# Performance work log

Measured on AMD Instinct MI355X. Metric: run time of the kernel, lower is better.

The kernel has to match this reference:

```python
import jax, jax.numpy as jnp
import numpy as np

N_S = 50000   # support points
N_Q = 50000   # query points
H = 32        # neighbors per query
K = 15        # kernel points
C_IN = 64
C_OUT = 64
G = 8         # group norm groups
RADIUS = 1.0
SIGMA = 0.6
EPS = 1e-5
NEG_SLOPE = 0.1


def setup_inputs() -> dict:
    key = jax.random.key(0)
    ks = jax.random.split(key, 8)
    s_feats = jax.random.normal(ks[0], (N_S, C_IN), jnp.float32)
    q_points = jax.random.uniform(ks[1], (N_Q, 3), jnp.float32)
    s_points = jax.random.uniform(ks[2], (N_S, 3), jnp.float32)
    # index N_S is the shadow (padding) neighbor
    neighbor_indices = jax.random.randint(ks[3], (N_Q, H), 0, N_S + 1)
    # kernel point dispositions: fixed points inside a ball of RADIUS
    d = jax.random.normal(ks[4], (K, 3), jnp.float32)
    d = d / jnp.linalg.norm(d, axis=1, keepdims=True)
    r = jax.random.uniform(ks[5], (K, 1), jnp.float32) ** (1.0 / 3.0)
    kernel_points = d * r * RADIUS                      # (K,3)
    weights = jax.random.normal(ks[6], (K, C_IN, C_OUT), jnp.float32) * (1.0 / np.sqrt(K * C_IN))
    bias = jax.random.normal(ks[7], (C_OUT,), jnp.float32) * 0.01
    gamma = jnp.ones((C_OUT,), jnp.float32)
    beta = jnp.zeros((C_OUT,), jnp.float32)
    return dict(s_feats=s_feats, q_points=q_points, s_points=s_points,
                neighbor_indices=neighbor_indices, kernel_points=kernel_points,
                weights=weights, bias=bias, gamma=gamma, beta=beta)


def kpconv(s_feats, q_points, s_points, neighbor_indices, kernel_points, weights, bias):
    # pad support set with shadow point (1e10) and zero features
    pad_pts = jnp.concatenate([s_points, jnp.full((1, 3), 1e10, s_points.dtype)], axis=0)
    pad_feats = jnp.concatenate([s_feats, jnp.zeros((1, s_feats.shape[1]), s_feats.dtype)], axis=0)
    nbr_pts = pad_pts[neighbor_indices] - q_points[:, None, :]              # (M,H,3)
    diff = nbr_pts[:, :, None, :] - kernel_points[None, None, :, :]         # (M,H,K,3)
    sq_d = jnp.sum(diff * diff, axis=-1)                                    # (M,H,K)
    # linear correlation influence, clamped at 0
    w = jnp.maximum(1.0 - jnp.sqrt(sq_d) / SIGMA, 0.0)                      # (M,H,K)
    nbr_feats = pad_feats[neighbor_indices]                                 # (M,H,Cin)
    weighted = jnp.einsum('mhk,mhc->mkc', w, nbr_feats)                     # (M,K,Cin)
    out = jnp.einsum('mkc,kcd->md', weighted, weights)                      # (M,Cout)
    # normalize by number of valid neighbors (feature-sum > 0 test, as in KPConv)
    nbr_num = jnp.sum(jnp.sum(nbr_feats, axis=-1) > 0, axis=-1)             # (M,)
    nbr_num = jnp.maximum(nbr_num, 1).astype(out.dtype)
    return out / nbr_num[:, None] + bias


def group_norm(x, gamma, beta):
    # matches GroupNorm wrapper: (M,C) -> (1,C,M) -> nn.GroupNorm -> (M,C)
    M, C = x.shape
    xg = x.T.reshape(G, C // G, M)                                          # (G,Cg,M)
    mean = xg.mean(axis=(1, 2), keepdims=True)
    var = xg.var(axis=(1, 2), keepdims=True)
    xn = ((xg - mean) / jnp.sqrt(var + EPS)).reshape(C, M).T                # (M,C)
    return xn * gamma + beta


def reference(s_feats, q_points, s_points, neighbor_indices, kernel_points, weights, bias, gamma, beta):
    x = kpconv(s_feats, q_points, s_points, neighbor_indices, kernel_points, weights, bias)
    x = group_norm(x, gamma, beta)
    x = jnp.where(x >= 0, x, NEG_SLOPE * x)                                 # LeakyReLU(0.1)
    return x[:, None, :]                                                    # unsqueeze(1): (M,1,Cout)
```

## Files before the change

kernel.cpp:

```cpp
#include <hip/hip_runtime.h>
#include <hip/hip_bf16.h>
#include <math.h>

#define NSUP 50000
#define NQ   50000
#define NH   32
#define NK   15
#define NG   8
#define INV_SIGMA (1.0f/0.6f)
#define GN_EPS 1e-5f
#define NEG  0.1f

#define QB   16
#define NBLK (NQ/QB)

#define OFF_ROWSUM 0
#define OFF_FB     50048
#define OFF_WB     (OFF_FB + 1600000)
#define OFF_PS     (OFF_WB + 30720)
#define OFF_PQ     (OFF_PS + NBLK*8)

typedef __attribute__((ext_vector_type(8))) short bf16x8;
typedef __attribute__((ext_vector_type(4))) float f32x4;
typedef __attribute__((ext_vector_type(4))) unsigned int u32x4;

__device__ __forceinline__ short f2bf(float x) {
    __hip_bfloat16 h = __float2bfloat16(x);
    return *reinterpret_cast<short*>(&h);
}

__global__ __launch_bounds__(256) void k_prep(const float* __restrict__ sf,
                                              float* __restrict__ rowsum,
                                              unsigned short* __restrict__ fb,
                                              const float* __restrict__ wts,
                                              unsigned short* __restrict__ wb) {
    if (blockIdx.x < 3125) {
        const int lane = threadIdx.x & 63;
        const int row  = blockIdx.x * 16 + (threadIdx.x >> 6) * 4 + (lane >> 4);
        const int c4   = lane & 15;
        const float4 v = ((const float4*)sf)[(size_t)row * 16 + c4];
        ushort4 b;
        b.x = (unsigned short)f2bf(v.x); b.y = (unsigned short)f2bf(v.y);
        b.z = (unsigned short)f2bf(v.z); b.w = (unsigned short)f2bf(v.w);
        *(ushort4*)&fb[(size_t)row * 64 + c4 * 4] = b;
        float s = v.x + v.y + v.z + v.w;
        #pragma unroll
        for (int o = 1; o <= 8; o <<= 1) s += __shfl_xor(s, o);
        if (c4 == 0) rowsum[row] = s;
    } else {
        int idx = (blockIdx.x - 3125) * 256 + threadIdx.x;
        if (idx >= 30 * 4 * 64 * 8) return;
        int j  = idx & 7;
        int l  = (idx >> 3) & 63;
        int n  = (idx >> 9) & 3;
        int ks = idx >> 11;
        int r  = ks * 32 + ((l >> 4) << 3) + j;
        int d  = n * 16 + (l & 15);
        wb[idx] = (unsigned short)f2bf(wts[(size_t)r * 64 + d]);
    }
}

__global__ __launch_bounds__(256, 5) void k_conv(
    const unsigned short* __restrict__ fb, const float* __restrict__ qpts,
    const float* __restrict__ spts,  const int*   __restrict__ nidx,
    const float* __restrict__ kpts,  const unsigned short* __restrict__ wb,
    const float* __restrict__ bias,  const float* __restrict__ rowsum,
    float* __restrict__ conv_out, float* __restrict__ part_s, float* __restrict__ part_q)
{
    __shared__ __align__(16) short wl16[16 * 968];
    __shared__ __align__(16) float kp4[16][4];
    __shared__ float rcl[16];

    const int tid  = threadIdx.x;
    const int wv   = tid >> 6;
    const int lane = tid & 63;
    const int g    = lane >> 4;
    const int c16  = lane & 15;

    if (tid < 16) {
        if (tid < NK) {
            kp4[tid][0] = kpts[tid*3+0];
            kp4[tid][1] = kpts[tid*3+1];
            kp4[tid][2] = kpts[tid*3+2];
        } else {
            kp4[tid][0] = 1e8f; kp4[tid][1] = 1e8f; kp4[tid][2] = 1e8f;
        }
        kp4[tid][3] = 0.f;
    }
    __syncthreads();

    const float kx = kp4[c16][0], ky = kp4[c16][1], kz = kp4[c16][2];

    const int qbase = blockIdx.x * QB;
    char*  WV  = (char*)wl16 + wv * 7424;
    float* XYP = (float*)WV;
    char*  FP  = WV + 2560;

    f32x4 pacc[4][4];
    #pragma unroll
    for (int a = 0; a < 4; a++)
        #pragma unroll
        for (int b = 0; b < 4; b++) pacc[a][b] = (f32x4){0.f,0.f,0.f,0.f};

    const int h    = lane & 31;
    const int half = lane >> 5;

    #pragma unroll
    for (int pp = 0; pp < 2; pp++) {
        const int qq = pp*2 + half;
        const int m  = qbase + wv*4 + qq;
        const float qx = qpts[m*3+0], qy = qpts[m*3+1], qz = qpts[m*3+2];
        const int  id  = nidx[(size_t)m * NH + h];
        const bool val = (id < NSUP);
        const int  ii  = val ? id : 0;
        const float dx = spts[ii*3+0]-qx, dy = spts[ii*3+1]-qy, dz = spts[ii*3+2]-qz;
        const float rs = rowsum[ii];
        unsigned long long bal = __ballot(val && rs > 0.f);
        int cA = __popcll(bal & 0xffffffffull); if (cA < 1) cA = 1;
        int cB = __popcll(bal >> 32);           if (cB < 1) cB = 1;
        if (lane == 0)  rcl[wv*4 + pp*2]     = 1.0f / (float)cA;
        if (lane == 32) rcl[wv*4 + pp*2 + 1] = 1.0f / (float)cB;
        const int si = (pp*64 + half*32 + h) * 5;
        XYP[si]     = val ? dx : 1e10f;
        XYP[si + 1] = dy;
        XYP[si + 2] = dz;
    }

    const int gr = lane >> 3;
    const int gs = lane & 7;
    int   idA[4], idB[4];
    u32x4 vA[4], vB[4];
    {
        const int m0 = qbase + wv*4;
        #pragma unroll
        for (int i = 0; i < 4; i++) idA[i] = nidx[(size_t)m0*NH + i*8 + gr];
        #pragma unroll
        for (int i = 0; i < 4; i++) {
            const int id2 = (idA[i] < NSUP) ? idA[i] : 0;
            vA[i] = *(const u32x4*)((const char*)fb + (size_t)id2*128 + gs*16);
        }
        const int m1 = qbase + wv*4 + 1;
        #pragma unroll
        for (int i = 0; i < 4; i++) idB[i] = nidx[(size_t)m1*NH + i*8 + gr];
    }

    #pragma unroll
    for (int q = 0; q < 4; q++) {
        const int pp = q >> 1, e = q & 1;
        u32x4* vc  = (q & 1) ? vB  : vA;
        u32x4* vn  = (q & 1) ? vA  : vB;
        int*   idn = (q & 1) ? idA : idB;
        int*   idt = (q & 1) ? idB : idA;

        #pragma unroll
        for (int i = 0; i < 4; i++)
            *(u32x4*)(FP + (i*8 + gr)*144 + ((gs ^ i) << 4)) = vc[i];

        if (q < 3) {
            #pragma unroll
            for (int i = 0; i < 4; i++) {
                const int id2 = (idn[i] < NSUP) ? idn[i] : 0;
                vn[i] = *(const u32x4*)((const char*)fb + (size_t)id2*128 + gs*16);
            }
        }
        if (q < 2) {
            const int mn = qbase + wv*4 + q + 2;
            #pragma unroll
            for (int i = 0; i < 4; i++) idt[i] = nidx[(size_t)mn*NH + i*8 + gr];
        }

        union { unsigned short u[8]; bf16x8 v; } ua;
        #pragma unroll
        for (int j = 0; j < 8; j++) {
            const int xi = (pp*64 + e*32 + g*8 + j) * 5;
            const float px = XYP[xi], py = XYP[xi+1], pz = XYP[xi+2];
            const float ex = px - kx, ey = py - ky, ez = pz - kz;
            const float sq = fmaf(ex, ex, fmaf(ey, ey, ez * ez));
            const float w  = fmaxf(1.0f - sqrtf(sq) * INV_SIGMA, 0.f);
            ua.u[j] = (unsigned short)f2bf(w);
        }

        #pragma unroll
        for (int ct = 0; ct < 4; ct++) {
            const char* vb = FP + (g*8)*144
                           + (((((ct << 1) | (c16 >> 3)) ^ g) & 7) << 4)
                           + ((c16 & 7) << 1);
            union { unsigned short u[8]; bf16x8 v; } ub;
            #pragma unroll
            for (int j = 0; j < 8; j++)
                ub.u[j] = *(const unsigned short*)(vb + j*144);
            pacc[q][ct] = __builtin_amdgcn_mfma_f32_16x16x32_bf16(ua.v, ub.v, pacc[q][ct], 0, 0, 0);
        }
    }

    __syncthreads();

    #pragma unroll
    for (int qq = 0; qq < 4; qq++) {
        #pragma unroll
        for (int ct = 0; ct < 4; ct++) {
            #pragma unroll
            for (int i = 0; i < 4; i++) {
                const int kk = g*4 + i;
                if (kk < NK)
                    wl16[(wv*4 + qq)*968 + kk*64 + ct*16 + c16] = f2bf(pacc[qq][ct][i]);
            }
        }
    }
    __syncthreads();

    f32x4 facc = (f32x4){0.f,0.f,0.f,0.f};
    const int z = lane >> 4;
    const short* ap = wl16 + c16*968 + z*8;
    const unsigned short* bp = wb + ((size_t)(wv * 64 + lane)) * 8;
    #pragma unroll 6
    for (int ks = 0; ks < 30; ks++) {
        bf16x8 a = *(const bf16x8*)(ap + ks*32);
        bf16x8 b = *(const bf16x8*)(bp + (size_t)ks*2048);
        facc = __builtin_amdgcn_mfma_f32_16x16x32_bf16(a, b, facc, 0, 0, 0);
    }

    const int   d  = wv*16 + c16;
    const float bs = bias[d];
    float gl = 0.f, gq = 0.f;
    #pragma unroll
    for (int i = 0; i < 4; i++) {
        const int row = z*4 + i;
        const float y = facc[i] * rcl[row] + bs;
        conv_out[(size_t)(qbase + row)*64 + d] = y;
        gl += y;
        gq = fmaf(y, y, gq);
    }
    #pragma unroll
    for (int msk = 1; msk <= 4; msk <<= 1) { gl += __shfl_xor(gl, msk); gq += __shfl_xor(gq, msk); }
    gl += __shfl_xor(gl, 16); gq += __shfl_xor(gq, 16);
    gl += __shfl_xor(gl, 32); gq += __shfl_xor(gq, 32);
    if ((lane & 55) == 0) {
        const int grp = wv*2 + (lane >> 3);
        part_s[(size_t)blockIdx.x * 8 + grp] = gl;
        part_q[(size_t)blockIdx.x * 8 + grp] = gq;
    }
}

__global__ __launch_bounds__(256) void k_apply(float* __restrict__ out,
                                               const float* __restrict__ part_s,
                                               const float* __restrict__ part_q,
                                               const float* __restrict__ gamma,
                                               const float* __restrict__ beta) {
    __shared__ double ds[32][8], dq[32][8];
    __shared__ float st[16];
    const int t = threadIdx.x;

    {
        const int gg = t & 7, chunk = t >> 3;
        const int per = (NBLK + 31) / 32;
        int lo = chunk * per, hi = lo + per; if (hi > NBLK) hi = NBLK;
        double s0 = 0.0, s1 = 0.0, s2 = 0.0, s3 = 0.0;
        double q0 = 0.0, q1 = 0.0, q2 = 0.0, q3 = 0.0;
        int i = lo;
        for (; i + 3 < hi; i += 4) {
            s0 += (double)part_s[(size_t)(i+0) * 8 + gg];
            s1 += (double)part_s[(size_t)(i+1) * 8 + gg];
            s2 += (double)part_s[(size_t)(i+2) * 8 + gg];
            s3 += (double)part_s[(size_t)(i+3) * 8 + gg];
            q0 += (double)part_q[(size_t)(i+0) * 8 + gg];
            q1 += (double)part_q[(size_t)(i+1) * 8 + gg];
            q2 += (double)part_q[(size_t)(i+2) * 8 + gg];
            q3 += (double)part_q[(size_t)(i+3) * 8 + gg];
        }
        for (; i < hi; i++) {
            s0 += (double)part_s[(size_t)i * 8 + gg];
            q0 += (double)part_q[(size_t)i * 8 + gg];
        }
        ds[chunk][gg] = (s0 + s1) + (s2 + s3);
        dq[chunk][gg] = (q0 + q1) + (q2 + q3);
        __syncthreads();
        if (t < 8) {
            double S = 0.0, Q = 0.0;
            for (int cix = 0; cix < 32; cix++) { S += ds[cix][t]; Q += dq[cix][t]; }
            const double cnt = (double)(64 / NG) * (double)NQ;
            double mean = S / cnt;
            double var  = Q / cnt - mean * mean;
            st[t]     = (float)mean;
            st[8 + t] = (float)(1.0 / sqrt(var + (double)GN_EPS));
        }
        __syncthreads();
    }

    const int n4 = NQ * 64 / 4;
    for (int idx = blockIdx.x * 256 + t; idx < n4; idx += gridDim.x * 256) {
        float4 v = ((const float4*)out)[idx];
        const int c4 = idx & 15;
        const int g  = c4 >> 1;
        const float mean = st[g], istd = st[8 + g];
        const float4 ga = ((const float4*)gamma)[c4];
        const float4 be = ((const float4*)beta)[c4];
        float4 r;
        r.x = (v.x - mean) * istd * ga.x + be.x; r.x = r.x >= 0.f ? r.x : NEG * r.x;
        r.y = (v.y - mean) * istd * ga.y + be.y; r.y = r.y >= 0.f ? r.y : NEG * r.y;
        r.z = (v.z - mean) * istd * ga.z + be.z; r.z = r.z >= 0.f ? r.z : NEG * r.z;
        r.w = (v.w - mean) * istd * ga.w + be.w; r.w = r.w >= 0.f ? r.w : NEG * r.w;
        ((float4*)out)[idx] = r;
    }
}

extern "C" void kernel_launch(void* const* d_in, const int* in_sizes, int n_in,
                              void* d_out, int out_size, void* d_ws, size_t ws_size,
                              hipStream_t stream) {
    const float* sfeats = (const float*)d_in[0];
    const float* qpts   = (const float*)d_in[1];
    const float* spts   = (const float*)d_in[2];
    const int*   nidx   = (const int*)  d_in[3];
    const float* kpts   = (const float*)d_in[4];
    const float* wts    = (const float*)d_in[5];
    const float* bias   = (const float*)d_in[6];
    const float* gamma  = (const float*)d_in[7];
    const float* beta   = (const float*)d_in[8];

    float* ws = (float*)d_ws;
    float*          rowsum = ws + OFF_ROWSUM;
    unsigned short* fb     = (unsigned short*)(ws + OFF_FB);
    unsigned short* wb     = (unsigned short*)(ws + OFF_WB);
    float*          ps     = ws + OFF_PS;
    float*          pq     = ws + OFF_PQ;
    float*          out    = (float*)d_out;

    k_prep <<<dim3(3365), dim3(256), 0, stream>>>(sfeats, rowsum, fb, wts, wb);
    k_conv <<<dim3(NBLK), dim3(256), 0, stream>>>(fb, qpts, spts, nidx, kpts,
                                                  wb, bias, rowsum, out, ps, pq);
    k_apply<<<dim3(512),  dim3(256), 0, stream>>>(out, ps, pq, gamma, beta);
}
```

Baseline: 76.78 us.

## Deepen neighbor feature gather prefetch to triple buffering and widen apply grid

The neighbor-feature gather pipeline in the conv kernel moves from double to triple buffering. Feature loads for the first two queries are now issued before the point-geometry setup, so their latency overlaps with that work, and later gathers are issued two stages ahead. This raises register pressure through the extra vC and idC buffers, which could lower occupancy. The group-norm apply kernel launch also grows from 512 to 1280 blocks to spread work across more CUs.

```diff
diff --git a/kernel.cpp b/kernel.cpp
--- a/kernel.cpp
+++ b/kernel.cpp
@@ -104,6 +104,30 @@
 
     const int h    = lane & 31;
     const int half = lane >> 5;
+    const int gr   = lane >> 3;
+    const int gs   = lane & 7;
+
+    int   idA[4], idB[4], idC[4];
+    u32x4 vA[4], vB[4], vC[4];
+    {
+        const int m0 = qbase + wv*4;
+        #pragma unroll
+        for (int i = 0; i < 4; i++) idA[i] = nidx[(size_t)m0*NH + i*8 + gr];
+        #pragma unroll
+        for (int i = 0; i < 4; i++) idB[i] = nidx[(size_t)(m0+1)*NH + i*8 + gr];
+        #pragma unroll
+        for (int i = 0; i < 4; i++) {
+            const int id2 = (idA[i] < NSUP) ? idA[i] : 0;
+            vA[i] = *(const u32x4*)((const char*)fb + (size_t)id2*128 + gs*16);
+        }
+        #pragma unroll
+        for (int i = 0; i < 4; i++) {
+            const int id2 = (idB[i] < NSUP) ? idB[i] : 0;
+            vB[i] = *(const u32x4*)((const char*)fb + (size_t)id2*128 + gs*16);
+        }
+        #pragma unroll
+        for (int i = 0; i < 4; i++) idC[i] = nidx[(size_t)(m0+2)*NH + i*8 + gr];
+    }
 
     #pragma unroll
     for (int pp = 0; pp < 2; pp++) {
@@ -126,47 +150,31 @@
         XYP[si + 2] = dz;
     }
 
-    const int gr = lane >> 3;
-    const int gs = lane & 7;
-    int   idA[4], idB[4];
-    u32x4 vA[4], vB[4];
-    {
-        const int m0 = qbase + wv*4;
-        #pragma unroll
-        for (int i = 0; i < 4; i++) idA[i] = nidx[(size_t)m0*NH + i*8 + gr];
-        #pragma unroll
-        for (int i = 0; i < 4; i++) {
-            const int id2 = (idA[i] < NSUP) ? idA[i] : 0;
-            vA[i] = *(const u32x4*)((const char*)fb + (size_t)id2*128 + gs*16);
-        }
-        const int m1 = qbase + wv*4 + 1;
-        #pragma unroll
-        for (int i = 0; i < 4; i++) idB[i] = nidx[(size_t)m1*NH + i*8 + gr];
-    }
-
     #pragma unroll
     for (int q = 0; q < 4; q++) {
         const int pp = q >> 1, e = q & 1;
-        u32x4* vc  = (q & 1) ? vB  : vA;
-        u32x4* vn  = (q & 1) ? vA  : vB;
-        int*   idn = (q & 1) ? idA : idB;
-        int*   idt = (q & 1) ? idB : idA;
+        u32x4* vc = (q == 0) ? vA : (q == 1) ? vB : (q == 2) ? vC : vB;
 
         #pragma unroll
         for (int i = 0; i < 4; i++)
             *(u32x4*)(FP + (i*8 + gr)*144 + ((gs ^ i) << 4)) = vc[i];
 
-        if (q < 3) {
+        if (q == 0) {
             #pragma unroll
             for (int i = 0; i < 4; i++) {
-                const int id2 = (idn[i] < NSUP) ? idn[i] : 0;
-                vn[i] = *(const u32x4*)((const char*)fb + (size_t)id2*128 + gs*16);
+                const int id2 = (idC[i] < NSUP) ? idC[i] : 0;
+                vC[i] = *(const u32x4*)((const char*)fb + (size_t)id2*128 + gs*16);
             }
-        }
-        if (q < 2) {
-            const int mn = qbase + wv*4 + q + 2;
-            #pragma unroll
-            for (int i = 0; i < 4; i++) idt[i] = nidx[(size_t)mn*NH + i*8 + gr];
+            const int m3 = qbase + wv*4 + 3;
+            #pragma unroll
+            for (int i = 0; i < 4; i++) idA[i] = nidx[(size_t)m3*NH + i*8 + gr];
+        }
+        if (q == 1) {
+            #pragma unroll
+            for (int i = 0; i < 4; i++) {
+                const int id2 = (idA[i] < NSUP) ? idA[i] : 0;
+                vB[i] = *(const u32x4*)((const char*)fb + (size_t)id2*128 + gs*16);
+            }
         }
 
         union { unsigned short u[8]; bf16x8 v; } ua;
@@ -328,5 +336,5 @@
     k_prep <<<dim3(3365), dim3(256), 0, stream>>>(sfeats, rowsum, fb, wts, wb);
     k_conv <<<dim3(NBLK), dim3(256), 0, stream>>>(fb, qpts, spts, nidx, kpts,
                                                   wb, bias, rowsum, out, ps, pq);
-    k_apply<<<dim3(512),  dim3(256), 0, stream>>>(out, ps, pq, gamma, beta);
-}
+    k_apply<<<dim3(1280), dim3(256), 0, stream>>>(out, ps, pq, gamma, beta);
+}
```

After: 76.99 us. About the same (+0.3%).
